# Kernel optimization log

Measured on AMD Instinct MI355X. Metric: run time of the kernel, lower is better.

## Reference

```python
import jax, jax.numpy as jnp
import numpy as np

B, N, D, H, C = 16, 512, 256, 8, 16
DK = D // H  # per-head dim


def gelu(x):
    return jax.nn.gelu(x, approximate=False)  # torch F.gelu default (erf)


def mha(x, Wq, Wk, Wv, Wo):
    # x: [N, D] treated as a length-N token sequence; standard scaled-dot MHA
    n = x.shape[0]
    q = (x @ Wq).reshape(n, H, DK)
    k = (x @ Wk).reshape(n, H, DK)
    v = (x @ Wv).reshape(n, H, DK)
    scores = jnp.einsum('nhd,mhd->hnm', q, k) / jnp.sqrt(jnp.asarray(DK, x.dtype))
    attn = jax.nn.softmax(scores, axis=-1)
    out = jnp.einsum('hnm,mhd->nhd', attn, v).reshape(n, H * DK)
    return out @ Wo


def setup_inputs() -> dict:
    key = jax.random.key(0)
    ks = jax.random.split(key, 16)
    scale = 1.0 / np.sqrt(D)
    w = lambda i, shape: jax.random.normal(ks[i], shape, jnp.float32) * scale
    return {
        'embeddings': jax.random.normal(ks[0], (B, N, D), jnp.float32),
        'labels': jax.random.randint(ks[1], (B, N), 0, C),
        'Wq0': w(2, (D, D)), 'Wk0': w(3, (D, D)), 'Wv0': w(4, (D, D)), 'Wo0': w(5, (D, D)),
        'Wq1': w(6, (D, D)), 'Wk1': w(7, (D, D)), 'Wv1': w(8, (D, D)), 'Wo1': w(9, (D, D)),
        'res_W': w(10, (D, D)), 'res_b': jnp.zeros((D,), jnp.float32),
        'ff_W1': w(11, (2 * D, D)), 'ff_b1': jnp.zeros((D,), jnp.float32),
        'ff_W2': w(12, (D, D)), 'ff_b2': jnp.zeros((D,), jnp.float32),
    }


def reference(embeddings, labels, Wq0, Wk0, Wv0, Wo0, Wq1, Wk1, Wv1, Wo1,
              res_W, res_b, ff_W1, ff_b1, ff_W2, ff_b2):
    # one-hot class membership; torch.unique over randint labels == arange(C)
    onehot = (labels[..., None] == jnp.arange(C)).astype(jnp.float32)  # [B,N,C]

    def episode(e, m):
        # e: [N, D]  m: [N, C]
        x = mha(e, Wq0, Wk0, Wv0, Wo0)
        x = gelu(x)
        x = mha(x, Wq1, Wk1, Wv1, Wo1)
        aggr = gelu(jnp.mean(x, axis=0))          # [D]  set-level summary
        aggr = aggr @ res_W + res_b               # res_linear
        e2 = jnp.concatenate([jnp.broadcast_to(aggr, (N, D)), e], axis=1)  # [N,2D]
        e2 = gelu(e2)
        e2 = gelu(e2 @ ff_W1 + ff_b1) @ ff_W2 + ff_b2  # ff_linear -> [N,D]
        # pairwise sample similarities with self-exclusion
        S = e2 @ e2.T                              # [N,N]
        S = S * (1.0 - jnp.eye(N, dtype=S.dtype))
        counts = jnp.sum(m, axis=0)                # [C]
        norm = counts[None, :] - m                 # leave-one-out class size [N,C]
        return (S.T @ m) / norm                    # per-class masked mean -> [N,C]

    return jax.vmap(episode)(embeddings, onehot)
```

## Files before the change

kernel.cpp:

```cpp
#include <hip/hip_runtime.h>

#define BB 16
#define NN 512
#define DD 256
#define HH 8
#define CC 16

typedef unsigned short u16;
using short8 = __attribute__((ext_vector_type(8))) short;
using f32x4  = __attribute__((ext_vector_type(4))) float;

__device__ __forceinline__ float gelu_f(float x) {
    return 0.5f * x * (1.0f + erff(x * 0.70710678118654752f));
}
__device__ __forceinline__ u16 f2bf(float f) {
    unsigned int u = __float_as_uint(f);
    unsigned int r = u + 0x7FFFu + ((u >> 16) & 1u);
    return (u16)(r >> 16);
}
__device__ __forceinline__ void gld16(const u16* g, const u16* l) {
    __builtin_amdgcn_global_load_lds(
        (const __attribute__((address_space(1))) unsigned int*)g,
        (__attribute__((address_space(3))) unsigned int*)l, 16, 0, 0);
}

#define QSCALE 0.25505412f

template<int AFP32>
__global__ __launch_bounds__(256) void gemm_qkv128(
    const void* __restrict__ Av,
    const u16* __restrict__ W0, const u16* __restrict__ W1, const u16* __restrict__ W2,
    u16* __restrict__ O0, u16* __restrict__ O1, u16* __restrict__ O2)
{
    __shared__ __align__(16) u16 As[128 * 32];
    __shared__ __align__(16) u16 Bs[64 * 32];
    const int tid = threadIdx.x, wave = tid >> 6, lane = tid & 63;
    const int col = lane & 15, quad = lane >> 4;
    const int mbase = blockIdx.x * 128;
    const int sel = blockIdx.y >> 2;
    const int nbase = (blockIdx.y & 3) * 64;
    const u16* W = (sel == 0) ? W0 : ((sel == 1) ? W1 : W2);
    u16* O = (sel == 0) ? O0 : ((sel == 1) ? O1 : O2);
    const int srow = lane >> 2, skk = (lane & 3) * 8;
    const int mh = (wave & 1) * 64, nh = (wave >> 1) * 32;

    f32x4 acc[4][2];
#pragma unroll
    for (int i = 0; i < 4; ++i)
#pragma unroll
        for (int j = 0; j < 2; ++j) acc[i][j] = (f32x4){0.f, 0.f, 0.f, 0.f};

    for (int k0 = 0; k0 < DD; k0 += 32) {
        if (AFP32) {
            const float* Af = (const float*)Av;
            const int row = tid >> 1, half = tid & 1;
            const float* src = Af + (size_t)(mbase + row) * DD + k0 + half * 16;
            ushort4 w0, w1, w2, w3;
            float4 v;
            v = *(const float4*)(src + 0);
            w0.x = f2bf(v.x); w0.y = f2bf(v.y); w0.z = f2bf(v.z); w0.w = f2bf(v.w);
            v = *(const float4*)(src + 4);
            w1.x = f2bf(v.x); w1.y = f2bf(v.y); w1.z = f2bf(v.z); w1.w = f2bf(v.w);
            v = *(const float4*)(src + 8);
            w2.x = f2bf(v.x); w2.y = f2bf(v.y); w2.z = f2bf(v.z); w2.w = f2bf(v.w);
            v = *(const float4*)(src + 12);
            w3.x = f2bf(v.x); w3.y = f2bf(v.y); w3.z = f2bf(v.z); w3.w = f2bf(v.w);
            *(ushort4*)&As[row * 32 + half * 16 + 0]  = w0;
            *(ushort4*)&As[row * 32 + half * 16 + 4]  = w1;
            *(ushort4*)&As[row * 32 + half * 16 + 8]  = w2;
            *(ushort4*)&As[row * 32 + half * 16 + 12] = w3;
        } else {
            const u16* Ab = (const u16*)Av;
#pragma unroll
            for (int c = 0; c < 2; ++c) {
                const int ch = wave * 2 + c;
                gld16(Ab + (size_t)(mbase + ch * 16 + srow) * DD + k0 + skk, &As[ch * 512]);
            }
        }
        gld16(W + (size_t)(nbase + wave * 16 + srow) * DD + k0 + skk, &Bs[wave * 512]);
        __syncthreads();
        short8 af[4], bfr[2];
#pragma unroll
        for (int i = 0; i < 4; ++i) af[i]  = *(const short8*)&As[(mh + i * 16 + col) * 32 + quad * 8];
#pragma unroll
        for (int j = 0; j < 2; ++j) bfr[j] = *(const short8*)&Bs[(nh + j * 16 + col) * 32 + quad * 8];
#pragma unroll
        for (int i = 0; i < 4; ++i)
#pragma unroll
            for (int j = 0; j < 2; ++j)
                acc[i][j] = __builtin_amdgcn_mfma_f32_16x16x32_bf16(af[i], bfr[j], acc[i][j], 0, 0, 0);
        __syncthreads();
    }

    const int b = mbase >> 9;
#pragma unroll
    for (int i = 0; i < 4; ++i) {
#pragma unroll
        for (int j = 0; j < 2; ++j) {
            const int ccol = nbase + nh + j * 16 + col;
            const int tok0 = (mbase & 511) + mh + i * 16 + quad * 4;
            const int head = ccol >> 5, dk = ccol & 31;
            if (sel == 2) {
                ushort4 pk;
                pk.x = f2bf(acc[i][j][0]); pk.y = f2bf(acc[i][j][1]);
                pk.z = f2bf(acc[i][j][2]); pk.w = f2bf(acc[i][j][3]);
                *(ushort4*)&O[(((size_t)b * HH + head) * 32 + dk) * NN + tok0] = pk;
            } else {
#pragma unroll
                for (int r = 0; r < 4; ++r) {
                    float v = acc[i][j][r];
                    if (sel == 0) v *= QSCALE;
                    O[(((size_t)b * HH + head) * NN + tok0 + r) * 32 + dk] = f2bf(v);
                }
            }
        }
    }
}

template<int ACT, int HAS_B, int HAS_T, int OUT_F32, int AG>
__global__ __launch_bounds__(256) void gemm64(
    const void* __restrict__ Av, const u16* __restrict__ W,
    u16* __restrict__ O, float* __restrict__ OF,
    const float* __restrict__ bias, const float* __restrict__ tvec)
{
    __shared__ __align__(16) u16 As[64 * 32];
    __shared__ __align__(16) u16 Bs[64 * 32];
    const int tid = threadIdx.x, wave = tid >> 6, lane = tid & 63;
    const int col = lane & 15, quad = lane >> 4;
    const int mbase = blockIdx.x * 64;
    const int nbase = blockIdx.y * 64;
    const int srow = lane >> 2, skk = (lane & 3) * 8;
    const int mh = (wave & 1) * 32, nh = (wave >> 1) * 32;

    f32x4 acc[2][2];
#pragma unroll
    for (int i = 0; i < 2; ++i)
#pragma unroll
        for (int j = 0; j < 2; ++j) acc[i][j] = (f32x4){0.f, 0.f, 0.f, 0.f};

    for (int k0 = 0; k0 < DD; k0 += 32) {
        if (AG) {
            const float* Af = (const float*)Av;
            const int row = tid >> 2, kq = tid & 3;
            const float* src = Af + (size_t)(mbase + row) * DD + k0 + kq * 8;
            float4 v0 = *(const float4*)(src + 0);
            float4 v1 = *(const float4*)(src + 4);
            ushort4 w0, w1;
            w0.x = f2bf(gelu_f(v0.x)); w0.y = f2bf(gelu_f(v0.y));
            w0.z = f2bf(gelu_f(v0.z)); w0.w = f2bf(gelu_f(v0.w));
            w1.x = f2bf(gelu_f(v1.x)); w1.y = f2bf(gelu_f(v1.y));
            w1.z = f2bf(gelu_f(v1.z)); w1.w = f2bf(gelu_f(v1.w));
            *(ushort4*)&As[row * 32 + kq * 8 + 0] = w0;
            *(ushort4*)&As[row * 32 + kq * 8 + 4] = w1;
        } else {
            const u16* Ab = (const u16*)Av;
            gld16(Ab + (size_t)(mbase + wave * 16 + srow) * DD + k0 + skk, &As[wave * 512]);
        }
        gld16(W + (size_t)(nbase + wave * 16 + srow) * DD + k0 + skk, &Bs[wave * 512]);
        __syncthreads();
        short8 af[2], bfr[2];
#pragma unroll
        for (int i = 0; i < 2; ++i) af[i]  = *(const short8*)&As[(mh + i * 16 + col) * 32 + quad * 8];
#pragma unroll
        for (int j = 0; j < 2; ++j) bfr[j] = *(const short8*)&Bs[(nh + j * 16 + col) * 32 + quad * 8];
#pragma unroll
        for (int i = 0; i < 2; ++i)
#pragma unroll
            for (int j = 0; j < 2; ++j)
                acc[i][j] = __builtin_amdgcn_mfma_f32_16x16x32_bf16(af[i], bfr[j], acc[i][j], 0, 0, 0);
        __syncthreads();
    }

    const int b = mbase >> 9;
#pragma unroll
    for (int i = 0; i < 2; ++i) {
#pragma unroll
        for (int j = 0; j < 2; ++j) {
            const int ccol = nbase + nh + j * 16 + col;
#pragma unroll
            for (int r = 0; r < 4; ++r) {
                const int crow = mbase + mh + i * 16 + quad * 4 + r;
                float v = acc[i][j][r];
                if (HAS_B) v += bias[ccol];
                if (HAS_T) v += tvec[b * DD + ccol];
                if (ACT)   v = gelu_f(v);
                if (OUT_F32) OF[(size_t)crow * DD + ccol] = v;
                else         O[(size_t)crow * DD + ccol] = f2bf(v);
            }
        }
    }
}

template<int COLSUM>
__global__ __launch_bounds__(256, 4) void attn_mfma(
    const u16* __restrict__ Qh, const u16* __restrict__ Kh,
    const u16* __restrict__ VT, u16* __restrict__ O,
    float* __restrict__ partial)
{
    __shared__ __align__(16) u16 Pc[4][16 * 40];
    __shared__ float cs[4][32];
    const int tid = threadIdx.x, wave = tid >> 6, lane = tid & 63;
    const int col = lane & 15, quad = lane >> 4;
    const int gid = blockIdx.x;
    const int qb = gid >> 7, bh = gid & 127;
    const int q0 = qb * 64 + wave * 16;

    const short8 aq = *(const short8*)(Qh + ((size_t)bh * NN + q0 + col) * 32 + quad * 8);
    const u16* ksrc = Kh + (size_t)bh * NN * 32;
    const u16* vsrc = VT + (size_t)bh * 32 * NN;

    float l[4] = {0.f, 0.f, 0.f, 0.f};
    f32x4 oacc[2];
    oacc[0] = (f32x4){0.f, 0.f, 0.f, 0.f};
    oacc[1] = (f32x4){0.f, 0.f, 0.f, 0.f};

    u16* pw = &Pc[wave][0];

#pragma unroll 4
    for (int g = 0; g < 16; ++g) {
#pragma unroll
        for (int k2 = 0; k2 < 2; ++k2) {
            const int kt = g * 2 + k2;
            const short8 bk = *(const short8*)(ksrc + (size_t)(kt * 16 + col) * 32 + quad * 8);
            f32x4 z = {0.f, 0.f, 0.f, 0.f};
            const f32x4 s = __builtin_amdgcn_mfma_f32_16x16x32_bf16(aq, bk, z, 0, 0, 0);
#pragma unroll
            for (int r = 0; r < 4; ++r) {
                const float p = exp2f(s[r]);
                l[r] += p;
                pw[(quad * 4 + r) * 40 + k2 * 16 + col] = f2bf(p);
            }
        }
        const short8 ap = *(const short8*)&pw[col * 40 + quad * 8];
#pragma unroll
        for (int nt = 0; nt < 2; ++nt) {
            const short8 bv = *(const short8*)(vsrc + (size_t)(nt * 16 + col) * NN + g * 32 + quad * 8);
            oacc[nt] = __builtin_amdgcn_mfma_f32_16x16x32_bf16(ap, bv, oacc[nt], 0, 0, 0);
        }
    }
#pragma unroll
    for (int r = 0; r < 4; ++r) {
        l[r] += __shfl_xor(l[r], 1, 64);
        l[r] += __shfl_xor(l[r], 2, 64);
        l[r] += __shfl_xor(l[r], 4, 64);
        l[r] += __shfl_xor(l[r], 8, 64);
    }
    if (COLSUM) {
        float sv[2] = {0.f, 0.f};
#pragma unroll
        for (int nt = 0; nt < 2; ++nt) {
#pragma unroll
            for (int r = 0; r < 4; ++r) sv[nt] += oacc[nt][r] / l[r];
            sv[nt] += __shfl_xor(sv[nt], 16, 64);
            sv[nt] += __shfl_xor(sv[nt], 32, 64);
        }
        if (lane < 16) { cs[wave][col] = sv[0]; cs[wave][16 + col] = sv[1]; }
        __syncthreads();
        if (tid < 32)
            partial[(size_t)(bh * 8 + qb) * 32 + tid] =
                cs[0][tid] + cs[1][tid] + cs[2][tid] + cs[3][tid];
    } else {
        const int b = bh >> 3, h = bh & 7;
        u16* obase = O + ((size_t)b * NN) * DD + h * 32;
#pragma unroll
        for (int nt = 0; nt < 2; ++nt)
#pragma unroll
            for (int r = 0; r < 4; ++r)
                obase[(size_t)(q0 + quad * 4 + r) * DD + nt * 16 + col] = f2bf(oacc[nt][r] / l[r]);
    }
}

__global__ __launch_bounds__(256) void convert_w(
    const float* s0, const float* s1, const float* s2, const float* s3,
    const float* s4, const float* s5, const float* s6, const float* s7,
    const float* s8, u16* __restrict__ Wt)
{
    const int w = blockIdx.x;
    const int my = w >> 4, kb = (w & 15) * 16;
    const int n = threadIdx.x;
    const float* S;
    switch (my) {
        case 0: S = s0; break; case 1: S = s1; break; case 2: S = s2; break;
        case 3: S = s3; break; case 4: S = s4; break; case 5: S = s5; break;
        case 6: S = s6; break; case 7: S = s7; break; default: S = s8; break;
    }
    u16* Dst = Wt + (size_t)my * 65536;
    for (int r = 0; r < 16; ++r) {
        const int k = kb + r;
        Dst[(size_t)n * 256 + k] = f2bf(S[(size_t)k * 256 + n]);
    }
}

__device__ __forceinline__ float mv256(const float* __restrict__ a,
                                       const float* __restrict__ W, int d)
{
    float acc[8] = {0.f, 0.f, 0.f, 0.f, 0.f, 0.f, 0.f, 0.f};
    for (int k = 0; k < 256; k += 8) {
#pragma unroll
        for (int j = 0; j < 8; ++j)
            acc[j] += a[k + j] * W[(size_t)(k + j) * 256 + d];
    }
    return ((acc[0] + acc[1]) + (acc[2] + acc[3])) + ((acc[4] + acc[5]) + (acc[6] + acc[7]));
}

__global__ __launch_bounds__(256) void aggr_v2(
    const float* __restrict__ partial, const float* __restrict__ Wo1f,
    const float* __restrict__ resW, const float* __restrict__ resb,
    const float* __restrict__ W1, const int* __restrict__ labels,
    float* __restrict__ tvec, float* __restrict__ counts)
{
    const int b = blockIdx.x, d = threadIdx.x;
    __shared__ float a0[256], a1[256], a2[256];
    __shared__ int hist[CC];
    if (d < CC) hist[d] = 0;
    const int h = d >> 5, d32 = d & 31;
    float s = 0.f;
#pragma unroll
    for (int qb = 0; qb < 8; ++qb)
        s += partial[(size_t)(((b * 8 + h) * 8) + qb) * 32 + d32];
    a0[d] = s * (1.0f / NN);
    __syncthreads();
    atomicAdd(&hist[labels[b * NN + d]], 1);
    atomicAdd(&hist[labels[b * NN + 256 + d]], 1);
    a1[d] = gelu_f(mv256(a0, Wo1f, d));
    __syncthreads();
    a2[d] = gelu_f(mv256(a1, resW, d) + resb[d]);
    __syncthreads();
    tvec[b * 256 + d] = mv256(a2, W1, d);
    if (d < CC) counts[b * CC + d] = (float)hist[d];
}

__global__ __launch_bounds__(256) void classsum_v2(
    const float* __restrict__ F, const int* __restrict__ labels,
    float* __restrict__ g)
{
    const int b = blockIdx.x, dch = blockIdx.y;
    const int t = threadIdx.x, w = t >> 6, lane = t & 63;
    __shared__ int lab[NN];
    __shared__ float gs[4][CC][64];
    lab[t] = labels[b * NN + t];
    lab[t + 256] = labels[b * NN + t + 256];
    __syncthreads();
    float acc[CC];
#pragma unroll
    for (int c = 0; c < CC; ++c) acc[c] = 0.f;
    const float* Fb = F + (size_t)b * NN * DD + dch * 64 + lane;
#pragma unroll 4
    for (int n = w * 128; n < w * 128 + 128; ++n) {
        const float v = Fb[(size_t)n * DD];
        const int lb = lab[n];
#pragma unroll
        for (int c = 0; c < CC; ++c) acc[c] += (lb == c) ? v : 0.f;
    }
#pragma unroll
    for (int c = 0; c < CC; ++c) gs[w][c][lane] = acc[c];
    __syncthreads();
#pragma unroll
    for (int i = 0; i < 4; ++i) {
        const int c = w * 4 + i;
        g[((size_t)b * CC + c) * DD + dch * 64 + lane] =
            gs[0][c][lane] + gs[1][c][lane] + gs[2][c][lane] + gs[3][c][lane];
    }
}

__global__ __launch_bounds__(256) void out_kernel(
    const float* __restrict__ F, const int* __restrict__ labels,
    const float* __restrict__ g, const float* __restrict__ counts,
    float* __restrict__ out)
{
    const int b = blockIdx.y;
    const int wave = threadIdx.x >> 6, lane = threadIdx.x & 63;
    const int n = blockIdx.x * 4 + wave;
    const float* fn = F + ((size_t)b * NN + n) * DD;
    const float* gb = g + (size_t)b * CC * DD;
    float fv[4];
#pragma unroll
    for (int i = 0; i < 4; ++i) fv[i] = fn[lane * 4 + i];
    float selfdot = 0.f;
#pragma unroll
    for (int i = 0; i < 4; ++i) selfdot += fv[i] * fv[i];
    float accs[CC];
#pragma unroll
    for (int c = 0; c < CC; ++c) {
        float sacc = 0.f;
#pragma unroll
        for (int i = 0; i < 4; ++i) sacc += fv[i] * gb[c * DD + lane * 4 + i];
        accs[c] = sacc;
    }
    for (int off = 32; off; off >>= 1) {
        selfdot += __shfl_xor(selfdot, off, 64);
#pragma unroll
        for (int c = 0; c < CC; ++c) accs[c] += __shfl_xor(accs[c], off, 64);
    }
    if (lane < CC) {
        const int c = lane;
        const int same = (labels[b * NN + n] == c) ? 1 : 0;
        const float num = accs[c] - (same ? selfdot : 0.f);
        const float den = counts[b * CC + c] - (float)same;
        out[((size_t)b * NN + n) * CC + c] = num / den;
    }
}

extern "C" void kernel_launch(void* const* d_in, const int* in_sizes, int n_in,
                              void* d_out, int out_size, void* d_ws, size_t ws_size,
                              hipStream_t stream)
{
    const float* emb    = (const float*)d_in[0];
    const int*   labels = (const int*)  d_in[1];
    const float* Wo1f = (const float*)d_in[9];
    const float* resW = (const float*)d_in[10];
    const float* resb = (const float*)d_in[11];
    const float* ffW1 = (const float*)d_in[12];
    const float* ffb1 = (const float*)d_in[13];
    const float* ffb2 = (const float*)d_in[15];
    float* out = (float*)d_out;

    const size_t SBE = (size_t)BB * NN * DD;
    u16* BUF0 = (u16*)d_ws;
    u16* BUF2 = BUF0 + SBE;
    u16* BUF3 = BUF2 + SBE;
    u16* BUF4 = BUF3 + SBE;
    u16* BUF5 = BUF4 + SBE;
    u16* Wt   = BUF5 + SBE;
    float* F      = (float*)(Wt + 9 * 65536);
    float* tvec   = F + SBE;
    float* partial= tvec + BB * 256;
    float* gsum   = partial + 128 * 8 * 32;
    float* counts = gsum + (size_t)BB * CC * DD;

    convert_w<<<144, 256, 0, stream>>>(
        (const float*)d_in[2], (const float*)d_in[3], (const float*)d_in[4],
        (const float*)d_in[5], (const float*)d_in[6], (const float*)d_in[7],
        (const float*)d_in[8], ffW1 + 256 * 256, (const float*)d_in[14], Wt);
    gemm_qkv128<1><<<dim3(64, 12), 256, 0, stream>>>(
        emb, Wt, Wt + 65536, Wt + 2 * 65536, BUF2, BUF3, BUF4);
    attn_mfma<0><<<1024, 256, 0, stream>>>(BUF2, BUF3, BUF4, BUF5, nullptr);
    gemm64<1,0,0,0,0><<<dim3(128, 4), 256, 0, stream>>>(
        BUF5, Wt + 3 * 65536, BUF0, nullptr, nullptr, nullptr);
    gemm_qkv128<0><<<dim3(64, 12), 256, 0, stream>>>(
        BUF0, Wt + 4 * 65536, Wt + 5 * 65536, Wt + 6 * 65536, BUF2, BUF3, BUF4);
    attn_mfma<1><<<1024, 256, 0, stream>>>(BUF2, BUF3, BUF4, nullptr, partial);
    aggr_v2<<<BB, 256, 0, stream>>>(partial, Wo1f, resW, resb, ffW1, labels, tvec, counts);
    gemm64<1,1,1,0,2><<<dim3(128, 4), 256, 0, stream>>>(
        emb, Wt + 7 * 65536, BUF3, nullptr, ffb1, tvec);
    gemm64<0,1,0,1,0><<<dim3(128, 4), 256, 0, stream>>>(
        BUF3, Wt + 8 * 65536, nullptr, F, ffb2, nullptr);
    classsum_v2<<<dim3(BB, 4), 256, 0, stream>>>(F, labels, gsum);
    out_kernel<<<dim3(128, BB), 256, 0, stream>>>(F, labels, gsum, counts, out);
}
```

Before: 237.8 us.

## Stage V tile in LDS for attention and coalesce fp32 A-tile loads

The attention kernel now copies the whole per-head V^T slice (32x512 bf16, padded rows) into shared memory at kernel start and reads its B fragments from LDS instead of global memory. The P scratch buffer loses its padding, and the min-occupancy launch bound and the unroll pragma are dropped. The two GEMM kernels remap the fp32 A-tile loads so consecutive threads read consecutive 8-float chunks, giving more coalesced global loads. The trade-off is higher LDS use per block, which may lower occupancy, and possible bank conflicts on the unpadded P buffer.

```diff
diff --git a/kernel.cpp b/kernel.cpp
--- a/kernel.cpp
+++ b/kernel.cpp
@@ -53,22 +53,19 @@
     for (int k0 = 0; k0 < DD; k0 += 32) {
         if (AFP32) {
             const float* Af = (const float*)Av;
-            const int row = tid >> 1, half = tid & 1;
-            const float* src = Af + (size_t)(mbase + row) * DD + k0 + half * 16;
-            ushort4 w0, w1, w2, w3;
-            float4 v;
-            v = *(const float4*)(src + 0);
-            w0.x = f2bf(v.x); w0.y = f2bf(v.y); w0.z = f2bf(v.z); w0.w = f2bf(v.w);
-            v = *(const float4*)(src + 4);
-            w1.x = f2bf(v.x); w1.y = f2bf(v.y); w1.z = f2bf(v.z); w1.w = f2bf(v.w);
-            v = *(const float4*)(src + 8);
-            w2.x = f2bf(v.x); w2.y = f2bf(v.y); w2.z = f2bf(v.z); w2.w = f2bf(v.w);
-            v = *(const float4*)(src + 12);
-            w3.x = f2bf(v.x); w3.y = f2bf(v.y); w3.z = f2bf(v.z); w3.w = f2bf(v.w);
-            *(ushort4*)&As[row * 32 + half * 16 + 0]  = w0;
-            *(ushort4*)&As[row * 32 + half * 16 + 4]  = w1;
-            *(ushort4*)&As[row * 32 + half * 16 + 8]  = w2;
-            *(ushort4*)&As[row * 32 + half * 16 + 12] = w3;
+#pragma unroll
+            for (int it = 0; it < 2; ++it) {
+                const int idx = tid * 8 + it * 2048;
+                const int row = idx >> 5, ko = idx & 31;
+                const float* src = Af + (size_t)(mbase + row) * DD + k0 + ko;
+                const float4 v0 = *(const float4*)(src + 0);
+                const float4 v1 = *(const float4*)(src + 4);
+                ushort4 w0, w1;
+                w0.x = f2bf(v0.x); w0.y = f2bf(v0.y); w0.z = f2bf(v0.z); w0.w = f2bf(v0.w);
+                w1.x = f2bf(v1.x); w1.y = f2bf(v1.y); w1.z = f2bf(v1.z); w1.w = f2bf(v1.w);
+                *(ushort4*)&As[idx + 0] = w0;
+                *(ushort4*)&As[idx + 4] = w1;
+            }
         } else {
             const u16* Ab = (const u16*)Av;
 #pragma unroll
@@ -141,17 +138,18 @@
     for (int k0 = 0; k0 < DD; k0 += 32) {
         if (AG) {
             const float* Af = (const float*)Av;
-            const int row = tid >> 2, kq = tid & 3;
-            const float* src = Af + (size_t)(mbase + row) * DD + k0 + kq * 8;
-            float4 v0 = *(const float4*)(src + 0);
-            float4 v1 = *(const float4*)(src + 4);
+            const int idx = tid * 8;
+            const int row = idx >> 5, ko = idx & 31;
+            const float* src = Af + (size_t)(mbase + row) * DD + k0 + ko;
+            const float4 v0 = *(const float4*)(src + 0);
+            const float4 v1 = *(const float4*)(src + 4);
             ushort4 w0, w1;
             w0.x = f2bf(gelu_f(v0.x)); w0.y = f2bf(gelu_f(v0.y));
             w0.z = f2bf(gelu_f(v0.z)); w0.w = f2bf(gelu_f(v0.w));
             w1.x = f2bf(gelu_f(v1.x)); w1.y = f2bf(gelu_f(v1.y));
             w1.z = f2bf(gelu_f(v1.z)); w1.w = f2bf(gelu_f(v1.w));
-            *(ushort4*)&As[row * 32 + kq * 8 + 0] = w0;
-            *(ushort4*)&As[row * 32 + kq * 8 + 4] = w1;
+            *(ushort4*)&As[idx + 0] = w0;
+            *(ushort4*)&As[idx + 4] = w1;
         } else {
             const u16* Ab = (const u16*)Av;
             gld16(Ab + (size_t)(mbase + wave * 16 + srow) * DD + k0 + skk, &As[wave * 512]);
@@ -192,12 +190,13 @@
 }
 
 template<int COLSUM>
-__global__ __launch_bounds__(256, 4) void attn_mfma(
+__global__ __launch_bounds__(256) void attn_mfma(
     const u16* __restrict__ Qh, const u16* __restrict__ Kh,
     const u16* __restrict__ VT, u16* __restrict__ O,
     float* __restrict__ partial)
 {
-    __shared__ __align__(16) u16 Pc[4][16 * 40];
+    __shared__ __align__(16) u16 Vt[32 * 520];
+    __shared__ __align__(16) u16 Pc[4][16 * 32];
     __shared__ float cs[4][32];
     const int tid = threadIdx.x, wave = tid >> 6, lane = tid & 63;
     const int col = lane & 15, quad = lane >> 4;
@@ -205,18 +204,21 @@
     const int qb = gid >> 7, bh = gid & 127;
     const int q0 = qb * 64 + wave * 16;
 
+    const u16* vsrc = VT + (size_t)bh * 32 * NN;
+#pragma unroll
+    for (int i = 0; i < 8; ++i) {
+        const int row = wave + i * 4;
+        gld16(vsrc + (size_t)row * NN + lane * 8, &Vt[row * 520]);
+    }
     const short8 aq = *(const short8*)(Qh + ((size_t)bh * NN + q0 + col) * 32 + quad * 8);
+    __syncthreads();
+
     const u16* ksrc = Kh + (size_t)bh * NN * 32;
-    const u16* vsrc = VT + (size_t)bh * 32 * NN;
-
     float l[4] = {0.f, 0.f, 0.f, 0.f};
     f32x4 oacc[2];
     oacc[0] = (f32x4){0.f, 0.f, 0.f, 0.f};
     oacc[1] = (f32x4){0.f, 0.f, 0.f, 0.f};
 
-    u16* pw = &Pc[wave][0];
-
-#pragma unroll 4
     for (int g = 0; g < 16; ++g) {
 #pragma unroll
         for (int k2 = 0; k2 < 2; ++k2) {
@@ -228,13 +230,13 @@
             for (int r = 0; r < 4; ++r) {
                 const float p = exp2f(s[r]);
                 l[r] += p;
-                pw[(quad * 4 + r) * 40 + k2 * 16 + col] = f2bf(p);
+                Pc[wave][(quad * 4 + r) * 32 + k2 * 16 + col] = f2bf(p);
             }
         }
-        const short8 ap = *(const short8*)&pw[col * 40 + quad * 8];
+        const short8 ap = *(const short8*)&Pc[wave][col * 32 + quad * 8];
 #pragma unroll
         for (int nt = 0; nt < 2; ++nt) {
-            const short8 bv = *(const short8*)(vsrc + (size_t)(nt * 16 + col) * NN + g * 32 + quad * 8);
+            const short8 bv = *(const short8*)&Vt[(nt * 16 + col) * 520 + g * 32 + quad * 8];
             oacc[nt] = __builtin_amdgcn_mfma_f32_16x16x32_bf16(ap, bv, oacc[nt], 0, 0, 0);
         }
     }
```

Measured after the change: 223.3 us. 6.1% less time.
